# Kernel optimization log

Hardware: AMD Instinct MI355X
Metric: run time of the kernel (lower is better)

Reference implementation:

```python
import jax, jax.numpy as jnp
import numpy as np

D_MODEL = 1024
NUM_HEADS = 16
D_K = D_MODEL // NUM_HEADS
C = 1.0  # Poincare ball curvature (MANIFOLD = PoincareBall(c=Curvature(1.0)))
EPS = 1e-15


def poincare_fully_connected(x, z, r, c):
    """hypll Poincare-ball fully connected layer (HNN++, Shimizu et al.).
    x: [..., in], z: [in, out], r: [out]. Returns a point in the ball, [..., out]."""
    c_sqrt = jnp.sqrt(c)
    lam = 2.0 / (1.0 - c * jnp.sum(x * x, axis=-1, keepdims=True))  # [..., 1]
    z_norm = jnp.maximum(jnp.linalg.norm(z, axis=0), EPS)  # [out]
    two_cr = 2.0 * c_sqrt * r  # [out]
    inner = x @ (z / z_norm)  # [..., out]
    # signed hyperplane distances v_k, then map back into the ball
    v = (2.0 * z_norm / c_sqrt) * jnp.arcsinh(
        c_sqrt * lam * inner * jnp.cosh(two_cr) - (lam - 1.0) * jnp.sinh(two_cr)
    )
    w = jnp.sinh(c_sqrt * v) / c_sqrt
    return w / (1.0 + jnp.sqrt(1.0 + c * jnp.sum(w * w, axis=-1, keepdims=True)))


def setup_inputs() -> dict:
    key = jax.random.key(0)
    ks = jax.random.split(key, 7)
    B, S, D = 4, 2048, D_MODEL
    x = jax.random.normal(ks[0], (B, S, D), jnp.float32)
    # place every token strictly inside the unit Poincare ball (max norm 0.7)
    x = 0.7 * x / jnp.max(jnp.linalg.norm(x, axis=-1, keepdims=True))
    scale = 1.0 / np.sqrt(D).astype(np.float32)
    return {
        "x": x,
        "z_q": jax.random.normal(ks[1], (D, D), jnp.float32) * scale,
        "b_q": jax.random.normal(ks[2], (D,), jnp.float32) * 0.01,
        "z_k": jax.random.normal(ks[3], (D, D), jnp.float32) * scale,
        "b_k": jax.random.normal(ks[4], (D,), jnp.float32) * 0.01,
        "w_v": jax.random.normal(ks[5], (D, D), jnp.float32) * scale,
        "b_v": jax.random.normal(ks[6], (D,), jnp.float32) * 0.01,
    }


def reference(x, z_q, b_q, z_k, b_k, w_v, b_v):
    B, S, D = x.shape
    Q = poincare_fully_connected(x, z_q, b_q, C)  # [B,S,D] hyperbolic projection
    K = poincare_fully_connected(x, z_k, b_k, C)  # [B,S,D]
    V = x @ w_v.T + b_v                            # [B,S,D] Euclidean nn.Linear

    def split_heads(t):  # [B,S,D] -> [B,H,S,Dk]
        return t.reshape(B, S, NUM_HEADS, D_K).transpose(0, 2, 1, 3)

    Qh, Kh, Vh = split_heads(Q), split_heads(K), split_heads(V)
    scores = jnp.einsum("bhqd,bhkd->bhqk", Qh, Kh) / np.sqrt(D_K).astype(np.float32)
    probs = jax.nn.softmax(scores, axis=-1)
    out = jnp.einsum("bhqk,bhkd->bhqd", probs, Vh)  # [B,H,S,Dk]
    return out.transpose(0, 2, 1, 3).reshape(B, S, D)
```

## Files before the change

### kernel.cpp

```cpp
#include <hip/hip_runtime.h>
#include <hip/hip_bf16.h>
#include <math.h>

#define D_MODEL 1024
#define NHEADS  16
#define DKH     64
#define BATCH   4
#define SEQ     2048
#define NTOK    (BATCH * SEQ)
#define NELEM   ((size_t)NTOK * D_MODEL)

typedef __bf16 v8bf __attribute__((ext_vector_type(8)));
typedef float  v4f  __attribute__((ext_vector_type(4)));

__device__ __forceinline__ v8bf ld_bf16x8(const ushort* p) {
    union { uint4 u; v8bf b; } cv;
    cv.u = *(const uint4*)p;
    return cv.b;
}
__device__ __forceinline__ ushort f2bf(float f) {
    __hip_bfloat16 h = __float2bfloat16(f);
    return *(ushort*)&h;
}
__device__ __forceinline__ uint cvt_pk_bf16(float lo, float hi) {
    uint r;
    asm("v_cvt_pk_bf16_f32 %0, %1, %2" : "=v"(r) : "v"(lo), "v"(hi));
    return r;
}

#define GLOAD_LDS16(gsrc, ldst)                                            \
    __builtin_amdgcn_global_load_lds(                                      \
        (const __attribute__((address_space(1))) void*)(gsrc),             \
        (__attribute__((address_space(3))) void*)(ldst), 16, 0, 0)

__device__ __forceinline__ float block_reduce_sum(float v, float* sbuf) {
    #pragma unroll
    for (int off = 32; off > 0; off >>= 1)
        v += __shfl_xor(v, off, 64);
    int lane = threadIdx.x & 63;
    int wid  = threadIdx.x >> 6;
    if (lane == 0) sbuf[wid] = v;
    __syncthreads();
    float total = sbuf[0] + sbuf[1] + sbuf[2] + sbuf[3];
    __syncthreads();
    return total;
}

__global__ __launch_bounds__(256) void prep_kernel2(const float* __restrict__ z_q,
                                                    const float* __restrict__ r_q,
                                                    const float* __restrict__ z_k,
                                                    const float* __restrict__ r_k,
                                                    float* __restrict__ aux) {
    __shared__ float sbuf[4];
    const float* z = blockIdx.y ? z_k : z_q;
    const float* r = blockIdx.y ? r_k : r_q;
    float* base = aux + blockIdx.y * 3072;
    int m = blockIdx.x;
    float s = 0.f;
    for (int k = threadIdx.x; k < D_MODEL; k += 256) {
        float zv = z[k * D_MODEL + m];
        s += zv * zv;
    }
    float tot = block_reduce_sum(s, sbuf);
    if (threadIdx.x == 0) {
        float n = fmaxf(sqrtf(tot), 1e-15f);
        float tc = 2.f * r[m];
        base[m]        = coshf(tc) / n;
        base[1024 + m] = sinhf(tc);
        base[2048 + m] = 2.f * n;
    }
}

__global__ __launch_bounds__(256) void cast_x_lam(const float* __restrict__ x,
                                                  ushort* __restrict__ xb,
                                                  float* __restrict__ lam) {
    __shared__ float sbuf[4];
    int n = blockIdx.x;
    const float* xr = x + (size_t)n * D_MODEL;
    float4 v = *(const float4*)&xr[threadIdx.x * 4];
    float s = v.x * v.x + v.y * v.y + v.z * v.z + v.w * v.w;
    float xn2 = block_reduce_sum(s, sbuf);
    if (threadIdx.x == 0) lam[n] = 2.f / (1.f - xn2);
    ushort u[4] = {f2bf(v.x), f2bf(v.y), f2bf(v.z), f2bf(v.w)};
    *(uint2*)&xb[(size_t)n * D_MODEL + threadIdx.x * 4] = *(uint2*)u;
}

__global__ __launch_bounds__(256) void cast_bf16(const float* __restrict__ in,
                                                 ushort* __restrict__ out) {
    size_t i = ((size_t)blockIdx.x * 256 + threadIdx.x) * 8;
    float4 a = *(const float4*)(in + i);
    float4 b = *(const float4*)(in + i + 4);
    ushort u[8] = {f2bf(a.x), f2bf(a.y), f2bf(a.z), f2bf(a.w),
                   f2bf(b.x), f2bf(b.y), f2bf(b.z), f2bf(b.w)};
    *(uint4*)(out + i) = *(uint4*)u;
}

__global__ __launch_bounds__(256) void cast_transpose2(const float* __restrict__ zq,
                                                       const float* __restrict__ zk,
                                                       ushort* __restrict__ zqT,
                                                       ushort* __restrict__ zkT) {
    __shared__ float tile[64][65];
    const float* z = blockIdx.z ? zk : zq;
    ushort* zT = blockIdx.z ? zkT : zqT;
    int t = threadIdx.x;
    int k0 = blockIdx.y * 64, m0 = blockIdx.x * 64;
    #pragma unroll
    for (int i = 0; i < 4; ++i) {
        int r = (t >> 4) + 16 * i;
        int c = (t & 15) * 4;
        float4 v = *(const float4*)&z[(size_t)(k0 + r) * D_MODEL + m0 + c];
        tile[r][c + 0] = v.x; tile[r][c + 1] = v.y;
        tile[r][c + 2] = v.z; tile[r][c + 3] = v.w;
    }
    __syncthreads();
    #pragma unroll
    for (int i = 0; i < 2; ++i) {
        int idx = t + 256 * i;
        int r = idx >> 3;
        int c8 = idx & 7;
        ushort u[8];
        #pragma unroll
        for (int j = 0; j < 8; ++j)
            u[j] = f2bf(tile[c8 * 8 + j][r]);
        *(uint4*)&zT[(size_t)(m0 + r) * D_MODEL + k0 + c8 * 8] = *(uint4*)u;
    }
}

__global__ __launch_bounds__(256) void gemm_fused(const ushort* __restrict__ A,
                                                  const ushort* __restrict__ W,
                                                  const float* __restrict__ bias,
                                                  float* __restrict__ Pq,
                                                  float* __restrict__ Pk,
                                                  ushort* __restrict__ VT) {
    const int K = 1024;
    __shared__ ushort As[128][64];
    __shared__ ushort Bs[128][64];
    int tid = threadIdx.x;
    int w = tid >> 6, l = tid & 63;
    int lr = l & 15, lg = l >> 4;
    int wr = w >> 1, wc = w & 1;
    int bid = blockIdx.x;
    int xcd = bid & 7, t = bid >> 3;
    int m0 = (xcd * 8 + t / 24) * 128;
    int n0 = (t % 24) * 128;

    v4f acc[4][4];
    #pragma unroll
    for (int i = 0; i < 4; ++i)
        #pragma unroll
        for (int j = 0; j < 4; ++j)
            acc[i][j] = (v4f){0.f, 0.f, 0.f, 0.f};

    int srow = w * 32 + (l >> 3);
    int scol = (l & 7) * 8;

    for (int k0 = 0; k0 < K; k0 += 64) {
        #pragma unroll
        for (int j = 0; j < 4; ++j) {
            GLOAD_LDS16(A + (size_t)(m0 + srow + j * 8) * K + k0 + scol,
                        &As[w * 32 + j * 8][0]);
            GLOAD_LDS16(W + (size_t)(n0 + srow + j * 8) * K + k0 + scol,
                        &Bs[w * 32 + j * 8][0]);
        }
        __syncthreads();
        #pragma unroll
        for (int kk = 0; kk < 2; ++kk) {
            v8bf av[4], bv[4];
            #pragma unroll
            for (int i = 0; i < 4; ++i)
                av[i] = *(const v8bf*)&As[wr * 64 + i * 16 + lr][kk * 32 + lg * 8];
            #pragma unroll
            for (int j = 0; j < 4; ++j)
                bv[j] = *(const v8bf*)&Bs[wc * 64 + j * 16 + lr][kk * 32 + lg * 8];
            #pragma unroll
            for (int i = 0; i < 4; ++i)
                #pragma unroll
                for (int j = 0; j < 4; ++j)
                    acc[i][j] = __builtin_amdgcn_mfma_f32_16x16x32_bf16(av[i], bv[j], acc[i][j], 0, 0, 0);
        }
        __syncthreads();
    }

    int chunk = n0 >> 10;
    #pragma unroll
    for (int i = 0; i < 4; ++i) {
        #pragma unroll
        for (int j = 0; j < 4; ++j) {
            int col = n0 + wc * 64 + j * 16 + lr;
            int cl  = col & 1023;
            if (chunk == 0) {
                #pragma unroll
                for (int reg = 0; reg < 4; ++reg) {
                    int row = m0 + wr * 64 + i * 16 + 4 * lg + reg;
                    Pq[(size_t)row * D_MODEL + cl] = acc[i][j][reg];
                }
            } else if (chunk == 1) {
                #pragma unroll
                for (int reg = 0; reg < 4; ++reg) {
                    int row = m0 + wr * 64 + i * 16 + 4 * lg + reg;
                    Pk[(size_t)row * D_MODEL + cl] = acc[i][j][reg];
                }
            } else {
                float badd = bias[cl];
                int hh = cl >> 6, dk = cl & 63;
                int row = m0 + wr * 64 + i * 16 + 4 * lg;
                int bb = row >> 11, ss = row & 2047;
                int sp = (ss & ~63) | (ss & 0x23) | ((ss & 0x0C) << 1) | ((ss & 0x10) >> 2);
                ushort u[4];
                #pragma unroll
                for (int reg = 0; reg < 4; ++reg)
                    u[reg] = f2bf(acc[i][j][reg] + badd);
                *(uint2*)&VT[(((size_t)(bb * NHEADS + hh)) * DKH + dk) * SEQ + sp] = *(uint2*)u;
            }
        }
    }
}

__global__ __launch_bounds__(256) void poincare_epilogue2(const float* __restrict__ Pq,
                                                          const float* __restrict__ Pk,
                                                          const float* __restrict__ lam_,
                                                          const float* __restrict__ aux,
                                                          ushort* __restrict__ Qb,
                                                          ushort* __restrict__ Kb) {
    __shared__ float sbuf[4];
    int which = blockIdx.y;
    const float* P   = which ? Pk : Pq;
    ushort* outb     = which ? Kb : Qb;
    const float* c1_ = aux + which * 3072;
    const float* sh_ = c1_ + 1024;
    const float* tz_ = c1_ + 2048;
    float oscale = which ? 1.0f : 0.1803368801f;

    int n = blockIdx.x;
    float lam = lam_[n];
    float lm1 = lam - 1.f;
    int o = threadIdx.x * 4;
    float4 p  = *(const float4*)&P[(size_t)n * D_MODEL + o];
    float4 c1 = *(const float4*)&c1_[o];
    float4 sh = *(const float4*)&sh_[o];
    float4 tz = *(const float4*)&tz_[o];
    float pv[4]  = {p.x, p.y, p.z, p.w};
    float c1v[4] = {c1.x, c1.y, c1.z, c1.w};
    float shv[4] = {sh.x, sh.y, sh.z, sh.w};
    float tzv[4] = {tz.x, tz.y, tz.z, tz.w};
    float w[4];
    float wn2 = 0.f;
    #pragma unroll
    for (int i = 0; i < 4; ++i) {
        float t  = fmaf(lam * c1v[i], pv[i], -lm1 * shv[i]);
        float at = fabsf(t);
        float u  = at + __builtin_amdgcn_sqrtf(fmaf(at, at, 1.f));
        float tl = tzv[i] * __builtin_amdgcn_logf(u);
        float e  = __builtin_amdgcn_exp2f(tl);
        float em = __builtin_amdgcn_exp2f(-tl);
        float wa = 0.5f * (e - em);
        w[i] = copysignf(wa, t);
        wn2 = fmaf(wa, wa, wn2);
    }
    wn2 = block_reduce_sum(wn2, sbuf);
    float invd = oscale / (1.f + __builtin_amdgcn_sqrtf(1.f + wn2));
    uint2 st;
    st.x = cvt_pk_bf16(w[0] * invd, w[1] * invd);
    st.y = cvt_pk_bf16(w[2] * invd, w[3] * invd);
    *(uint2*)&outb[(size_t)n * D_MODEL + o] = st;
}

__global__ __launch_bounds__(512, 4) void attn_mfma(const ushort* __restrict__ Qb,
                                                    const ushort* __restrict__ Kb,
                                                    const ushort* __restrict__ VT,
                                                    float* __restrict__ Out) {
    __shared__ ushort Klds[4][64 * 64];
    __shared__ ushort Vlds[4][64 * 64];

    int tid = threadIdx.x;
    int w = tid >> 6, l = tid & 63;
    int lr = l & 15, lg = l >> 4;

    int flat = blockIdx.x;
    int low3 = flat & 7;
    int rest = flat >> 3;
    int qx   = rest & 7;
    int g    = (rest & ~7) | low3;
    int h = g & 15, b = g >> 4;

    const ushort* Kh = Kb + (size_t)b * SEQ * D_MODEL + h * DKH;
    const ushort* Vh = VT + (size_t)(b * NHEADS + h) * DKH * SEQ;

    const ushort* qp0 = Qb + (size_t)b * SEQ * D_MODEL + h * DKH
                      + (size_t)(qx * 256 + w * 32 + lr) * D_MODEL;
    const ushort* qp1 = qp0 + (size_t)16 * D_MODEL;
    v8bf qa[2][2];
    qa[0][0] = ld_bf16x8(qp0 + lg * 8);
    qa[0][1] = ld_bf16x8(qp0 + 32 + lg * 8);
    qa[1][0] = ld_bf16x8(qp1 + lg * 8);
    qa[1][1] = ld_bf16x8(qp1 + 32 + lg * 8);

    int row = tid >> 3;
    int c8  = (tid & 7) ^ (row & 7);
    const ushort* kg = Kh + (size_t)row * D_MODEL + c8 * 8;
    const ushort* vg = Vh + (size_t)row * SEQ + c8 * 8;

#define STAGE_KV(buf, st)  do {                                              \
        GLOAD_LDS16(kg + (size_t)(st) * 64 * D_MODEL, &Klds[buf][tid * 8]);  \
        GLOAD_LDS16(vg + (st) * 64, &Vlds[buf][tid * 8]);                    \
    } while (0)

    v4f o[2][4];
    v4f den4[2];
    #pragma unroll
    for (int st = 0; st < 2; ++st) {
        den4[st] = (v4f){0.f, 0.f, 0.f, 0.f};
        #pragma unroll
        for (int i = 0; i < 4; ++i) o[st][i] = (v4f){0.f, 0.f, 0.f, 0.f};
    }
    union { uint u[4]; v8bf v; } ones;
    ones.u[0] = ones.u[1] = ones.u[2] = ones.u[3] = 0x3f803f80u;

    auto compute = [&](int buf) {
        const char* Kc = (const char*)&Klds[buf][0];
        const char* Vc = (const char*)&Vlds[buf][0];

        v4f sc[2][4];
        #pragma unroll
        for (int st = 0; st < 2; ++st)
            #pragma unroll
            for (int i = 0; i < 4; ++i) sc[st][i] = (v4f){0.f, 0.f, 0.f, 0.f};
        __builtin_amdgcn_s_setprio(1);
        #pragma unroll
        for (int f = 0; f < 2; ++f) {
            #pragma unroll
            for (int sub = 0; sub < 4; ++sub) {
                int key = sub * 16 + lr;
                v8bf kb = *(const v8bf*)(Kc + key * 128 +
                                         ((f * 64 + lg * 16) ^ ((key & 7) << 4)));
                sc[0][sub] = __builtin_amdgcn_mfma_f32_16x16x32_bf16(kb, qa[0][f], sc[0][sub], 0, 0, 0);
                sc[1][sub] = __builtin_amdgcn_mfma_f32_16x16x32_bf16(kb, qa[1][f], sc[1][sub], 0, 0, 0);
            }
        }
        __builtin_amdgcn_s_setprio(0);

        uint pk[2][8];
        #pragma unroll
        for (int st = 0; st < 2; ++st) {
            #pragma unroll
            for (int sub = 0; sub < 4; ++sub) {
                float p0 = __builtin_amdgcn_exp2f(sc[st][sub][0]);
                float p1 = __builtin_amdgcn_exp2f(sc[st][sub][1]);
                float p2 = __builtin_amdgcn_exp2f(sc[st][sub][2]);
                float p3 = __builtin_amdgcn_exp2f(sc[st][sub][3]);
                pk[st][sub * 2 + 0] = cvt_pk_bf16(p0, p1);
                pk[st][sub * 2 + 1] = cvt_pk_bf16(p2, p3);
            }
        }

        __builtin_amdgcn_s_setprio(1);
        #pragma unroll
        for (int f = 0; f < 2; ++f) {
            union { uint u[4]; v8bf v; } pa0, pa1;
            #pragma unroll
            for (int j = 0; j < 4; ++j) { pa0.u[j] = pk[0][4 * f + j]; pa1.u[j] = pk[1][4 * f + j]; }
            den4[0] = __builtin_amdgcn_mfma_f32_16x16x32_bf16(pa0.v, ones.v, den4[0], 0, 0, 0);
            den4[1] = __builtin_amdgcn_mfma_f32_16x16x32_bf16(pa1.v, ones.v, den4[1], 0, 0, 0);
            #pragma unroll
            for (int sub = 0; sub < 4; ++sub) {
                int dk = sub * 16 + lr;
                v8bf vb = *(const v8bf*)(Vc + dk * 128 +
                                         ((f * 64 + lg * 16) ^ ((dk & 7) << 4)));
                o[0][sub] = __builtin_amdgcn_mfma_f32_16x16x32_bf16(pa0.v, vb, o[0][sub], 0, 0, 0);
                o[1][sub] = __builtin_amdgcn_mfma_f32_16x16x32_bf16(pa1.v, vb, o[1][sub], 0, 0, 0);
            }
        }
        __builtin_amdgcn_s_setprio(0);
    };

    STAGE_KV(0, 0);
    STAGE_KV(1, 1);
    STAGE_KV(2, 2);

    for (int tb = 0; tb < 28; tb += 4) {
        #pragma unroll
        for (int i = 0; i < 4; ++i) {
            asm volatile("s_waitcnt vmcnt(4)" ::: "memory");
            __syncthreads();
            STAGE_KV((i + 3) & 3, tb + i + 3);
            compute(i);
        }
    }
    asm volatile("s_waitcnt vmcnt(4)" ::: "memory");
    __syncthreads();
    STAGE_KV(3, 31);
    compute(0);
    asm volatile("s_waitcnt vmcnt(4)" ::: "memory");
    __syncthreads();
    compute(1);
    asm volatile("s_waitcnt vmcnt(2)" ::: "memory");
    __syncthreads();
    compute(2);
    asm volatile("s_waitcnt vmcnt(0)" ::: "memory");
    __syncthreads();
    compute(3);

    #pragma unroll
    for (int st = 0; st < 2; ++st) {
        size_t obase = (size_t)b * SEQ * D_MODEL +
                       (size_t)(qx * 256 + w * 32 + st * 16 + lg * 4) * D_MODEL + h * DKH;
        #pragma unroll
        for (int reg = 0; reg < 4; ++reg) {
            float inv = 1.f / den4[st][reg];
            #pragma unroll
            for (int sub = 0; sub < 4; ++sub)
                Out[obase + (size_t)reg * D_MODEL + sub * 16 + lr] = o[st][sub][reg] * inv;
        }
    }
#undef STAGE_KV
}

extern "C" void kernel_launch(void* const* d_in, const int* in_sizes, int n_in,
                              void* d_out, int out_size, void* d_ws, size_t ws_size,
                              hipStream_t stream) {
    const float* x   = (const float*)d_in[0];
    const float* z_q = (const float*)d_in[1];
    const float* b_q = (const float*)d_in[2];
    const float* z_k = (const float*)d_in[3];
    const float* b_k = (const float*)d_in[4];
    const float* w_v = (const float*)d_in[5];
    const float* b_v = (const float*)d_in[6];
    float* out = (float*)d_out;

    float*  Pq   = (float*)d_ws;
    ushort* xb   = (ushort*)(Pq + NELEM);
    ushort* Qb   = xb;
    ushort* Wcat = xb + NELEM;
    ushort* VT   = Wcat + (size_t)3 * D_MODEL * D_MODEL;
    ushort* Kb   = VT + NELEM;
    float*  aux  = (float*)(Kb + NELEM);
    float*  lam  = aux + 6144;
    float*  Pk   = out;

    prep_kernel2<<<dim3(1024, 2), 256, 0, stream>>>(z_q, b_q, z_k, b_k, aux);

    cast_x_lam<<<dim3(NTOK), 256, 0, stream>>>(x, xb, lam);
    cast_transpose2<<<dim3(16, 16, 2), 256, 0, stream>>>(z_q, z_k, Wcat,
                                                         Wcat + (size_t)D_MODEL * D_MODEL);
    cast_bf16<<<dim3(D_MODEL * D_MODEL / 8 / 256), 256, 0, stream>>>(
        w_v, Wcat + (size_t)2 * D_MODEL * D_MODEL);

    gemm_fused<<<dim3(1536), 256, 0, stream>>>(xb, Wcat, b_v, Pq, Pk, VT);

    poincare_epilogue2<<<dim3(NTOK, 2), 256, 0, stream>>>(Pq, Pk, lam, aux, Qb, Kb);

    attn_mfma<<<dim3(512), 512, 0, stream>>>(Qb, Kb, VT, out);
}
```

Before: 199.6 us.

## Double-buffer GEMM LDS loads, store Q/K pre-activations as bf16, use raw barriers

The fused projection GEMM now double-buffers its A/B LDS tiles, issuing the next k-step's loads before computing the current one and waiting with vmcnt. The block-to-tile mapping is reordered so each XCD works on 8x4 groups of tiles. The Q/K pre-activation buffers are written and read as bf16 instead of fp32, halving that intermediate traffic at some precision cost before the arcsinh/sinh epilogue. __syncthreads is replaced by raw s_barrier in the GEMM and attention loops to avoid the implicit waitcnt; this relies on the explicit vmcnt waits being correct.

```diff
diff --git a/kernel.cpp b/kernel.cpp
--- a/kernel.cpp
+++ b/kernel.cpp
@@ -32,6 +32,8 @@
     __builtin_amdgcn_global_load_lds(                                      \
         (const __attribute__((address_space(1))) void*)(gsrc),             \
         (__attribute__((address_space(3))) void*)(ldst), 16, 0, 0)
+
+#define RAW_BARRIER() __builtin_amdgcn_s_barrier()
 
 __device__ __forceinline__ float block_reduce_sum(float v, float* sbuf) {
     #pragma unroll
@@ -129,20 +131,20 @@
 __global__ __launch_bounds__(256) void gemm_fused(const ushort* __restrict__ A,
                                                   const ushort* __restrict__ W,
                                                   const float* __restrict__ bias,
-                                                  float* __restrict__ Pq,
-                                                  float* __restrict__ Pk,
+                                                  ushort* __restrict__ Pq,
+                                                  ushort* __restrict__ Pk,
                                                   ushort* __restrict__ VT) {
     const int K = 1024;
-    __shared__ ushort As[128][64];
-    __shared__ ushort Bs[128][64];
+    __shared__ ushort As[2][128][64];
+    __shared__ ushort Bs[2][128][64];
     int tid = threadIdx.x;
     int w = tid >> 6, l = tid & 63;
     int lr = l & 15, lg = l >> 4;
     int wr = w >> 1, wc = w & 1;
     int bid = blockIdx.x;
     int xcd = bid & 7, t = bid >> 3;
-    int m0 = (xcd * 8 + t / 24) * 128;
-    int n0 = (t % 24) * 128;
+    int m0 = (xcd * 8 + ((t >> 2) & 7)) * 128;
+    int n0 = ((t >> 5) * 4 + (t & 3)) * 128;
 
     v4f acc[4][4];
     #pragma unroll
@@ -154,32 +156,44 @@
     int srow = w * 32 + (l >> 3);
     int scol = (l & 7) * 8;
 
+#define STAGE_G(buf, k0) do {                                                 \
+        _Pragma("unroll")                                                     \
+        for (int j = 0; j < 4; ++j) {                                         \
+            GLOAD_LDS16(A + (size_t)(m0 + srow + j * 8) * K + (k0) + scol,    \
+                        &As[buf][w * 32 + j * 8][0]);                         \
+            GLOAD_LDS16(W + (size_t)(n0 + srow + j * 8) * K + (k0) + scol,    \
+                        &Bs[buf][w * 32 + j * 8][0]);                         \
+        }                                                                     \
+    } while (0)
+
+    STAGE_G(0, 0);
     for (int k0 = 0; k0 < K; k0 += 64) {
-        #pragma unroll
-        for (int j = 0; j < 4; ++j) {
-            GLOAD_LDS16(A + (size_t)(m0 + srow + j * 8) * K + k0 + scol,
-                        &As[w * 32 + j * 8][0]);
-            GLOAD_LDS16(W + (size_t)(n0 + srow + j * 8) * K + k0 + scol,
-                        &Bs[w * 32 + j * 8][0]);
-        }
-        __syncthreads();
+        int cur = (k0 >> 6) & 1;
+        if (k0 + 64 < K) {
+            STAGE_G(cur ^ 1, k0 + 64);
+            asm volatile("s_waitcnt vmcnt(8)" ::: "memory");
+        } else {
+            asm volatile("s_waitcnt vmcnt(0)" ::: "memory");
+        }
+        RAW_BARRIER();
         #pragma unroll
         for (int kk = 0; kk < 2; ++kk) {
             v8bf av[4], bv[4];
             #pragma unroll
             for (int i = 0; i < 4; ++i)
-                av[i] = *(const v8bf*)&As[wr * 64 + i * 16 + lr][kk * 32 + lg * 8];
+                av[i] = *(const v8bf*)&As[cur][wr * 64 + i * 16 + lr][kk * 32 + lg * 8];
             #pragma unroll
             for (int j = 0; j < 4; ++j)
-                bv[j] = *(const v8bf*)&Bs[wc * 64 + j * 16 + lr][kk * 32 + lg * 8];
+                bv[j] = *(const v8bf*)&Bs[cur][wc * 64 + j * 16 + lr][kk * 32 + lg * 8];
             #pragma unroll
             for (int i = 0; i < 4; ++i)
                 #pragma unroll
                 for (int j = 0; j < 4; ++j)
                     acc[i][j] = __builtin_amdgcn_mfma_f32_16x16x32_bf16(av[i], bv[j], acc[i][j], 0, 0, 0);
         }
-        __syncthreads();
-    }
+        RAW_BARRIER();
+    }
+#undef STAGE_G
 
     int chunk = n0 >> 10;
     #pragma unroll
@@ -188,17 +202,12 @@
         for (int j = 0; j < 4; ++j) {
             int col = n0 + wc * 64 + j * 16 + lr;
             int cl  = col & 1023;
-            if (chunk == 0) {
+            if (chunk < 2) {
+                ushort* P = chunk ? Pk : Pq;
                 #pragma unroll
                 for (int reg = 0; reg < 4; ++reg) {
                     int row = m0 + wr * 64 + i * 16 + 4 * lg + reg;
-                    Pq[(size_t)row * D_MODEL + cl] = acc[i][j][reg];
-                }
-            } else if (chunk == 1) {
-                #pragma unroll
-                for (int reg = 0; reg < 4; ++reg) {
-                    int row = m0 + wr * 64 + i * 16 + 4 * lg + reg;
-                    Pk[(size_t)row * D_MODEL + cl] = acc[i][j][reg];
+                    P[(size_t)row * D_MODEL + cl] = f2bf(acc[i][j][reg]);
                 }
             } else {
                 float badd = bias[cl];
@@ -216,15 +225,15 @@
     }
 }
 
-__global__ __launch_bounds__(256) void poincare_epilogue2(const float* __restrict__ Pq,
-                                                          const float* __restrict__ Pk,
+__global__ __launch_bounds__(256) void poincare_epilogue2(const ushort* __restrict__ Pq,
+                                                          const ushort* __restrict__ Pk,
                                                           const float* __restrict__ lam_,
                                                           const float* __restrict__ aux,
                                                           ushort* __restrict__ Qb,
                                                           ushort* __restrict__ Kb) {
     __shared__ float sbuf[4];
     int which = blockIdx.y;
-    const float* P   = which ? Pk : Pq;
+    const ushort* P  = which ? Pk : Pq;
     ushort* outb     = which ? Kb : Qb;
     const float* c1_ = aux + which * 3072;
     const float* sh_ = c1_ + 1024;
@@ -235,11 +244,15 @@
     float lam = lam_[n];
     float lm1 = lam - 1.f;
     int o = threadIdx.x * 4;
-    float4 p  = *(const float4*)&P[(size_t)n * D_MODEL + o];
+    uint2 pu = *(const uint2*)&P[(size_t)n * D_MODEL + o];
     float4 c1 = *(const float4*)&c1_[o];
     float4 sh = *(const float4*)&sh_[o];
     float4 tz = *(const float4*)&tz_[o];
-    float pv[4]  = {p.x, p.y, p.z, p.w};
+    float pv[4];
+    pv[0] = __uint_as_float(pu.x << 16);
+    pv[1] = __uint_as_float(pu.x & 0xffff0000u);
+    pv[2] = __uint_as_float(pu.y << 16);
+    pv[3] = __uint_as_float(pu.y & 0xffff0000u);
     float c1v[4] = {c1.x, c1.y, c1.z, c1.w};
     float shv[4] = {sh.x, sh.y, sh.z, sh.w};
     float tzv[4] = {tz.x, tz.y, tz.z, tz.w};
@@ -381,23 +394,23 @@
         #pragma unroll
         for (int i = 0; i < 4; ++i) {
             asm volatile("s_waitcnt vmcnt(4)" ::: "memory");
-            __syncthreads();
+            RAW_BARRIER();
             STAGE_KV((i + 3) & 3, tb + i + 3);
             compute(i);
         }
     }
     asm volatile("s_waitcnt vmcnt(4)" ::: "memory");
-    __syncthreads();
+    RAW_BARRIER();
     STAGE_KV(3, 31);
     compute(0);
     asm volatile("s_waitcnt vmcnt(4)" ::: "memory");
-    __syncthreads();
+    RAW_BARRIER();
     compute(1);
     asm volatile("s_waitcnt vmcnt(2)" ::: "memory");
-    __syncthreads();
+    RAW_BARRIER();
     compute(2);
     asm volatile("s_waitcnt vmcnt(0)" ::: "memory");
-    __syncthreads();
+    RAW_BARRIER();
     compute(3);
 
     #pragma unroll
@@ -427,15 +440,15 @@
     const float* b_v = (const float*)d_in[6];
     float* out = (float*)d_out;
 
-    float*  Pq   = (float*)d_ws;
-    ushort* xb   = (ushort*)(Pq + NELEM);
+    ushort* Pq   = (ushort*)d_ws;
+    ushort* xb   = Pq + NELEM;
     ushort* Qb   = xb;
     ushort* Wcat = xb + NELEM;
     ushort* VT   = Wcat + (size_t)3 * D_MODEL * D_MODEL;
     ushort* Kb   = VT + NELEM;
     float*  aux  = (float*)(Kb + NELEM);
     float*  lam  = aux + 6144;
-    float*  Pk   = out;
+    ushort* Pk   = (ushort*)out;
 
     prep_kernel2<<<dim3(1024, 2), 256, 0, stream>>>(z_q, b_q, z_k, b_k, aux);
 
```

Measured after the change: 187.5 us. 6.0% less time.
